# Kernel tuning notes

Measured on AMD Instinct MI355X. Metric: run time of the kernel, lower is better.

## Reference

```python
import jax, jax.numpy as jnp
import numpy as np

B, N, D = 2, 2048, 1024
H, HD = 16, 64            # num_heads, head_dim
INNER = H * HD
EPS = 1e-5


def setup_inputs() -> dict:
    key = jax.random.key(0)
    k0, k1, k2, k3 = jax.random.split(key, 4)
    x = jax.random.normal(k0, (B, N, D), dtype=jnp.float32)
    attn_mask = jax.random.randint(k1, (B, N, N), 0, 2, dtype=jnp.int32)
    gamma = jnp.ones((D,), jnp.float32)
    beta = jnp.zeros((D,), jnp.float32)
    w_qkv = jax.random.normal(k2, (D, 3 * INNER), dtype=jnp.float32) * 0.02
    w_out = jax.random.normal(k3, (INNER, D), dtype=jnp.float32) * 0.02
    b_out = jnp.zeros((D,), jnp.float32)
    return {"x": x, "attn_mask": attn_mask, "gamma": gamma, "beta": beta,
            "w_qkv": w_qkv, "w_out": w_out, "b_out": b_out}


def _rope_tables(n):
    # RotaryEmbedding buffers: sin/cos of shape [n, HD//2]
    inv_freq = 1.0 / (10000.0 ** (jnp.arange(0, HD, 2, dtype=jnp.float32) / HD))
    pos = jnp.arange(n, dtype=jnp.float32)
    ang = pos[:, None] * inv_freq[None, :]          # [n, HD//2]
    return jnp.sin(ang), jnp.cos(ang)


def _apply_rope(t, sin, cos):
    # t: [B, H, N, HD]; sin/cos broadcast as [1, 1, N, HD//2]
    t1, t2 = t[..., : HD // 2], t[..., HD // 2:]
    return jnp.concatenate([t1 * cos - t2 * sin, t2 * cos + t1 * sin], axis=-1)


def reference(x, attn_mask, gamma, beta, w_qkv, w_out, b_out):
    b, n, _ = x.shape
    # LayerNorm
    mu = jnp.mean(x, axis=-1, keepdims=True)
    var = jnp.mean(jnp.square(x - mu), axis=-1, keepdims=True)
    xn = (x - mu) * jax.lax.rsqrt(var + EPS) * gamma + beta
    # QKV projection (no bias)
    qkv = xn @ w_qkv                                 # [B, N, 3*INNER]
    q, k, v = jnp.split(qkv, 3, axis=-1)
    def to_heads(t):
        return t.reshape(b, n, H, HD).transpose(0, 2, 1, 3)  # [B, H, N, HD]
    q, k, v = to_heads(q), to_heads(k), to_heads(v)
    sin, cos = _rope_tables(n)
    sin = sin[None, None]                            # [1,1,N,HD//2]
    cos = cos[None, None]
    q = _apply_rope(q, sin, cos)
    k = _apply_rope(k, sin, cos)
    scale = HD ** -0.5
    scores = jnp.einsum('bhid,bhjd->bhij', q, k) * scale
    mask = (attn_mask > 0)[:, None, :, :]            # [B,1,N,N]
    scores = jnp.where(mask, scores, -jnp.inf)
    probs = jax.nn.softmax(scores, axis=-1)
    probs = jnp.nan_to_num(probs, nan=0.0)           # rows fully masked -> 0
    out = jnp.einsum('bhij,bhjd->bhid', probs, v)    # [B,H,N,HD]
    out = out.transpose(0, 2, 1, 3).reshape(b, n, INNER)
    return out @ w_out + b_out
```

## Files before the change

kernel.cpp:

```cpp
#include <hip/hip_runtime.h>
#include <stdint.h>
#include <math.h>

#define B_ 2
#define N_ 2048
#define D_ 1024
#define H_ 16
#define HD_ 64
#define TOK (B_*N_)
#define INNER_ (H_*HD_)

typedef unsigned short u16;
typedef __attribute__((ext_vector_type(8))) short bf16x8;
typedef __attribute__((ext_vector_type(4))) float f32x4;

__device__ __forceinline__ float bf2f(u16 u) {
  union { uint32_t i; float f; } v; v.i = ((uint32_t)u) << 16; return v.f;
}
__device__ __forceinline__ u16 f2bf(float f) {
  union { uint32_t i; float f; } v; v.f = f;
  uint32_t r = ((v.i >> 16) & 1u) + 0x7fffu;
  return (u16)((v.i + r) >> 16);
}
__device__ __forceinline__ uint32_t pk_bf16(float a, float b) {
  uint32_t ua = __float_as_uint(a) + 0x8000u;
  uint32_t ub = __float_as_uint(b) + 0x8000u;
  return __builtin_amdgcn_perm(ub, ua, 0x07060302);
}
__device__ __forceinline__ void gl_lds16(const void* g, void* l) {
  __builtin_amdgcn_global_load_lds(
      (const __attribute__((address_space(1))) uint32_t*)g,
      (__attribute__((address_space(3))) uint32_t*)l, 16, 0, 0);
}
__device__ __forceinline__ f32x4 mfma16(bf16x8 a, bf16x8 b, f32x4 c) {
  return __builtin_amdgcn_mfma_f32_16x16x32_bf16(a, b, c, 0, 0, 0);
}

__global__ void pack_mask(const int* __restrict__ mask, uint64_t* __restrict__ bits) {
  int t = threadIdx.x, lane = t & 63, w = t >> 6;
  int wi = blockIdx.x * 4 + w;
  int row = wi >> 5, jw = wi & 31;
  int m = mask[(size_t)row * 2048 + jw * 64 + lane];
  uint64_t bm = __ballot(m > 0);
  int b = row >> 11, i = row & 2047;
  if (lane == 0) bits[((size_t)(b * 32 + jw)) * 2048 + i] = bm;
}

__global__ void transpose_f2b(const float* __restrict__ in, u16* __restrict__ out,
                              int R, int C) {
  __shared__ u16 tile[64][65];
  int c0 = blockIdx.x * 64, r0 = blockIdx.y * 64;
  int t = threadIdx.x;
  int c = t & 63, r4 = t >> 6;
  for (int i = 0; i < 16; i++) {
    int r = r4 + i * 4;
    tile[c][r] = f2bf(in[(size_t)(r0 + r) * C + c0 + c]);
  }
  __syncthreads();
  int rr = t & 63, cc4 = t >> 6;
  for (int i = 0; i < 16; i++) {
    int cc = cc4 + i * 4;
    out[(size_t)(c0 + cc) * R + r0 + rr] = tile[cc][rr];
  }
}

__global__ void ln_kernel(const float* __restrict__ x, const float* __restrict__ gamma,
                          const float* __restrict__ beta, u16* __restrict__ xn) {
  int row = blockIdx.x, t = threadIdx.x;
  const float* xr = x + (size_t)row * D_;
  float4 u = *(const float4*)(xr + t * 4);
  float s = u.x + u.y + u.z + u.w;
  float ss = u.x * u.x + u.y * u.y + u.z * u.z + u.w * u.w;
  for (int off = 1; off < 64; off <<= 1) {
    s += __shfl_xor(s, off);
    ss += __shfl_xor(ss, off);
  }
  __shared__ float red[8];
  int wid = t >> 6, lane = t & 63;
  if (lane == 0) { red[wid] = s; red[wid + 4] = ss; }
  __syncthreads();
  s = red[0] + red[1] + red[2] + red[3];
  ss = red[4] + red[5] + red[6] + red[7];
  float mu = s * (1.0f / D_);
  float var = ss * (1.0f / D_) - mu * mu;
  float rinv = rsqrtf(var + 1e-5f);
  float4 g4 = *(const float4*)(gamma + t * 4);
  float4 b4 = *(const float4*)(beta + t * 4);
  ushort4 o;
  o.x = f2bf((u.x - mu) * rinv * g4.x + b4.x);
  o.y = f2bf((u.y - mu) * rinv * g4.y + b4.y);
  o.z = f2bf((u.z - mu) * rinv * g4.z + b4.z);
  o.w = f2bf((u.w - mu) * rinv * g4.w + b4.w);
  *(ushort4*)(xn + (size_t)row * D_ + t * 4) = o;
}

template<int FINAL>
__global__ void gemm_bt(const u16* __restrict__ A, const u16* __restrict__ Bt,
                        void* __restrict__ Cv, const float* __restrict__ bias,
                        int M, int N, int K) {
  __shared__ __align__(16) u16 As[128 * 64];
  __shared__ __align__(16) u16 Bs[128 * 64];
  const int t = threadIdx.x;
  const int lane = t & 63, wid = t >> 6;
  const int m0 = blockIdx.y * 128, n0 = blockIdx.x * 128;
  const int wm = (wid >> 1) * 64, wn = (wid & 1) * 64;
  const int l15 = lane & 15, quad = lane >> 4;

  f32x4 acc[4][4];
  const f32x4 zf = {0.f, 0.f, 0.f, 0.f};
  for (int i = 0; i < 4; i++) for (int j = 0; j < 4; j++) acc[i][j] = zf;

  for (int kb = 0; kb < K; kb += 64) {
    for (int i = 0; i < 4; i++) {
      int e = i * 256 + t;
      int row = e >> 3, gs = e & 7;
      int g = gs ^ (row & 7);
      gl_lds16(A + (size_t)(m0 + row) * K + kb + g * 8, &As[e * 8]);
      gl_lds16(Bt + (size_t)(n0 + row) * K + kb + g * 8, &Bs[e * 8]);
    }
    __syncthreads();
    bf16x8 af[4][2], bfr[4][2];
    for (int mt = 0; mt < 4; mt++)
      for (int kc = 0; kc < 2; kc++) {
        int row = wm + mt * 16 + l15;
        int gs = (kc * 4 + quad) ^ (row & 7);
        af[mt][kc] = *(const bf16x8*)&As[row * 64 + gs * 8];
      }
    for (int nt = 0; nt < 4; nt++)
      for (int kc = 0; kc < 2; kc++) {
        int row = wn + nt * 16 + l15;
        int gs = (kc * 4 + quad) ^ (row & 7);
        bfr[nt][kc] = *(const bf16x8*)&Bs[row * 64 + gs * 8];
      }
    for (int mt = 0; mt < 4; mt++)
      for (int nt = 0; nt < 4; nt++)
        for (int kc = 0; kc < 2; kc++)
          acc[mt][nt] = mfma16(af[mt][kc], bfr[nt][kc], acc[mt][nt]);
    __syncthreads();
  }
  for (int mt = 0; mt < 4; mt++)
    for (int nt = 0; nt < 4; nt++)
      for (int r = 0; r < 4; r++) {
        int row = m0 + wm + mt * 16 + quad * 4 + r;
        int col = n0 + wn + nt * 16 + l15;
        float v = acc[mt][nt][r];
        if (FINAL) {
          ((float*)Cv)[(size_t)row * N + col] = v + bias[col];
        } else {
          ((u16*)Cv)[(size_t)row * N + col] = f2bf(v);
        }
      }
}

__global__ void rope_kernel(const u16* __restrict__ qkv, u16* __restrict__ q,
                            u16* __restrict__ k, u16* __restrict__ vt) {
  int blk = blockIdx.x;
  int nt = blk & 31;
  int h = (blk >> 5) & 15;
  int b = blk >> 9;
  int n0 = nt * 64;
  int t = threadIdx.x;
  __shared__ u16 vs[64][65];
  const float QS = 0.125f * 1.4426950408889634f;
  for (int it = 0; it < 8; it++) {
    int idx = it * 256 + t;
    int i = idx >> 5, p = idx & 31;
    size_t base = (size_t)(b * 2048 + n0 + i) * 3072 + h * 64;
    float q1 = bf2f(qkv[base + p]),        q2 = bf2f(qkv[base + p + 32]);
    float k1 = bf2f(qkv[base + 1024 + p]), k2 = bf2f(qkv[base + 1024 + p + 32]);
    float pos = (float)(n0 + i);
    float inv = exp2f(-(float)p * (13.287712379549449f / 32.0f));
    float ang = pos * inv;
    float sn, cs;
    sincosf(ang, &sn, &cs);
    size_t qo = ((size_t)(b * 16 + h) * 2048 + n0 + i) * 64;
    q[qo + p]      = f2bf((q1 * cs - q2 * sn) * QS);
    q[qo + p + 32] = f2bf((q2 * cs + q1 * sn) * QS);
    k[qo + p]      = f2bf(k1 * cs - k2 * sn);
    k[qo + p + 32] = f2bf(k2 * cs + k1 * sn);
  }
  for (int it = 0; it < 16; it++) {
    int idx = it * 256 + t;
    int i = idx >> 6, d = idx & 63;
    vs[i][d] = qkv[(size_t)(b * 2048 + n0 + i) * 3072 + h * 64 + 2048 + d];
  }
  __syncthreads();
  for (int it = 0; it < 16; it++) {
    int idx = it * 256 + t;
    int d = idx >> 6, i = idx & 63;
    int c = i >> 5, hi = (i >> 4) & 1, qq = (i >> 2) & 3, r = i & 3;
    int slot = c * 32 + qq * 8 + hi * 4 + r;
    vt[((size_t)(b * 16 + h) * 64 + d) * 2048 + n0 + slot] = vs[i][d];
  }
}

__global__ __launch_bounds__(256, 4)
void attn_kernel(const u16* __restrict__ q, const u16* __restrict__ k,
                 const u16* __restrict__ vt, const uint64_t* __restrict__ bitsT,
                 u16* __restrict__ out) {
  int blk = blockIdx.x;
  int qt = blk & 31;
  int bh = blk >> 5;
  int b = bh >> 4, h = bh & 15;
  int q0 = qt * 64;
  int t = threadIdx.x, lane = t & 63, w = t >> 6;
  int l15 = lane & 15, quad = lane >> 4;

  __shared__ __align__(16) u16 sQ[64 * 64];
  __shared__ __align__(16) u16 sK[2][64 * 64];
  __shared__ __align__(16) u16 sV[2][64 * 64];

  {
    int e0 = t, e1 = 256 + t;
    int r0 = e0 >> 3, g0 = (e0 & 7) ^ (r0 & 7);
    int r1 = e1 >> 3, g1 = (e1 & 7) ^ (r1 & 7);
    gl_lds16(q + ((size_t)bh * 2048 + q0 + r0) * 64 + g0 * 8, &sQ[e0 * 8]);
    gl_lds16(q + ((size_t)bh * 2048 + q0 + r1) * 64 + g1 * 8, &sQ[e1 * 8]);
    gl_lds16(k + ((size_t)bh * 2048 + r0) * 64 + g0 * 8, &sK[0][e0 * 8]);
    gl_lds16(k + ((size_t)bh * 2048 + r1) * 64 + g1 * 8, &sK[0][e1 * 8]);
    gl_lds16(vt + ((size_t)bh * 64 + r0) * 2048 + g0 * 8, &sV[0][e0 * 8]);
    gl_lds16(vt + ((size_t)bh * 64 + r1) * 2048 + g1 * 8, &sV[0][e1 * 8]);
  }
  __syncthreads();

  bf16x8 bq[2];
  {
    int row = w * 16 + l15;
    for (int kc = 0; kc < 2; kc++) {
      int gs = (kc * 4 + quad) ^ (row & 7);
      bq[kc] = *(const bf16x8*)&sQ[row * 64 + gs * 8];
    }
  }

  const f32x4 zf = {0.f, 0.f, 0.f, 0.f};
  float l_i = 0.f;
  f32x4 acc_o[4];
  for (int dt = 0; dt < 4; dt++) acc_o[dt] = zf;
  const int qrow = q0 + w * 16 + l15;

  #pragma unroll 2
  for (int j64 = 0; j64 < 32; j64++) {
    if (j64) __syncthreads();
    int cur = j64 & 1;
    if (j64 + 1 < 32) {
      int nxt = cur ^ 1, j0n = (j64 + 1) * 64;
      int e0 = t, e1 = 256 + t;
      int r0 = e0 >> 3, g0 = (e0 & 7) ^ (r0 & 7);
      int r1 = e1 >> 3, g1 = (e1 & 7) ^ (r1 & 7);
      gl_lds16(k + ((size_t)bh * 2048 + j0n + r0) * 64 + g0 * 8, &sK[nxt][e0 * 8]);
      gl_lds16(k + ((size_t)bh * 2048 + j0n + r1) * 64 + g1 * 8, &sK[nxt][e1 * 8]);
      gl_lds16(vt + ((size_t)bh * 64 + r0) * 2048 + j0n + g0 * 8, &sV[nxt][e0 * 8]);
      gl_lds16(vt + ((size_t)bh * 64 + r1) * 2048 + j0n + g1 * 8, &sV[nxt][e1 * 8]);
    }
    const u16* sKc = sK[cur];
    const u16* sVc = sV[cur];

    uint64_t word = bitsT[((size_t)(b * 32 + j64)) * 2048 + qrow];
    uint64_t sh = word >> (quad * 4);
    uint32_t mlo = (uint32_t)sh, mhi = (uint32_t)(sh >> 32);

    float p[16];
    {
      f32x4 st[4];
      for (int jt = 0; jt < 4; jt++) {
        st[jt] = zf;
        int row = jt * 16 + l15;
        for (int kc = 0; kc < 2; kc++) {
          int gs = (kc * 4 + quad) ^ (row & 7);
          bf16x8 ak = *(const bf16x8*)&sKc[row * 64 + gs * 8];
          st[jt] = mfma16(ak, bq[kc], st[jt]);
        }
      }
      for (int jt = 0; jt < 4; jt++) {
        uint32_t mw = (jt & 2) ? mhi : mlo;
        int base = (jt & 1) * 16;
        for (int r = 0; r < 4; r++) {
          bool on = (mw >> (base + r)) & 1u;
          float e = exp2f(st[jt][r]);
          p[jt * 4 + r] = on ? e : 0.f;
        }
      }
    }
    float rsum = 0.f;
    for (int i = 0; i < 16; i++) rsum += p[i];
    rsum += __shfl_xor(rsum, 16);
    rsum += __shfl_xor(rsum, 32);
    l_i += rsum;

    for (int c = 0; c < 2; c++) {
      union { bf16x8 v; uint32_t d[4]; } bp;
      bp.d[0] = pk_bf16(p[(2 * c) * 4 + 0], p[(2 * c) * 4 + 1]);
      bp.d[1] = pk_bf16(p[(2 * c) * 4 + 2], p[(2 * c) * 4 + 3]);
      bp.d[2] = pk_bf16(p[(2 * c + 1) * 4 + 0], p[(2 * c + 1) * 4 + 1]);
      bp.d[3] = pk_bf16(p[(2 * c + 1) * 4 + 2], p[(2 * c + 1) * 4 + 3]);
      for (int dt = 0; dt < 4; dt++) {
        int drow = dt * 16 + l15;
        int gpos = (4 * c + quad) ^ (drow & 7);
        bf16x8 av = *(const bf16x8*)&sVc[drow * 64 + gpos * 8];
        acc_o[dt] = mfma16(av, bp.v, acc_o[dt]);
      }
    }
  }
  float rl = (l_i > 0.f) ? 1.0f / l_i : 0.f;
  size_t obase = ((size_t)b * 2048 + qrow) * 1024 + h * 64;
  for (int dt = 0; dt < 4; dt++) {
    ushort4 o;
    o.x = f2bf(acc_o[dt][0] * rl);
    o.y = f2bf(acc_o[dt][1] * rl);
    o.z = f2bf(acc_o[dt][2] * rl);
    o.w = f2bf(acc_o[dt][3] * rl);
    *(ushort4*)&out[obase + dt * 16 + quad * 4] = o;
  }
}

extern "C" void kernel_launch(void* const* d_in, const int* in_sizes, int n_in,
                              void* d_out, int out_size, void* d_ws, size_t ws_size,
                              hipStream_t stream) {
  const float* x = (const float*)d_in[0];
  const int* mask = (const int*)d_in[1];
  const float* gamma = (const float*)d_in[2];
  const float* beta = (const float*)d_in[3];
  const float* wqkv = (const float*)d_in[4];
  const float* wout = (const float*)d_in[5];
  const float* bout = (const float*)d_in[6];
  float* out = (float*)d_out;

  uint8_t* ws = (uint8_t*)d_ws;
  size_t o = 0;
  uint64_t* mbits = (uint64_t*)(ws + o); o += (size_t)TOK * 32 * 8;
  u16* wqkvT = (u16*)(ws + o); o += (size_t)3 * INNER_ * D_ * 2;
  u16* woutT = (u16*)(ws + o); o += (size_t)INNER_ * D_ * 2;
  u16* xn    = (u16*)(ws + o); o += (size_t)TOK * D_ * 2;
  u16* qkv   = (u16*)(ws + o); o += (size_t)TOK * 3 * INNER_ * 2;
  u16* kb    = (u16*)(ws + o); o += (size_t)TOK * INNER_ * 2;
  u16* vtb   = (u16*)(ws + o); o += (size_t)TOK * INNER_ * 2;
  u16* qb = xn;
  u16* ao = qkv;

  pack_mask<<<TOK * 32 / 4, 256, 0, stream>>>(mask, mbits);
  transpose_f2b<<<dim3(3 * INNER_ / 64, D_ / 64), 256, 0, stream>>>(wqkv, wqkvT, D_, 3 * INNER_);
  transpose_f2b<<<dim3(D_ / 64, INNER_ / 64), 256, 0, stream>>>(wout, woutT, INNER_, D_);
  ln_kernel<<<TOK, 256, 0, stream>>>(x, gamma, beta, xn);
  gemm_bt<0><<<dim3(3 * INNER_ / 128, TOK / 128), 256, 0, stream>>>(xn, wqkvT, qkv, nullptr, TOK, 3 * INNER_, D_);
  rope_kernel<<<B_ * H_ * (N_ / 64), 256, 0, stream>>>(qkv, qb, kb, vtb);
  attn_kernel<<<B_ * H_ * (N_ / 64), 256, 0, stream>>>(qb, kb, vtb, mbits, ao);
  gemm_bt<1><<<dim3(D_ / 128, TOK / 128), 256, 0, stream>>>(ao, woutT, out, bout, TOK, D_, INNER_);
}
```

Before: 257.3 us.

## Fuse RoPE and V transpose into QKV GEMM epilogue, double-buffer output GEMM

```diff
diff --git a/kernel.cpp b/kernel.cpp
--- a/kernel.cpp
+++ b/kernel.cpp
@@ -22,7 +22,10 @@
   uint32_t r = ((v.i >> 16) & 1u) + 0x7fffu;
   return (u16)((v.i + r) >> 16);
 }
-__device__ __forceinline__ uint32_t pk_bf16(float a, float b) {
+__device__ __forceinline__ uint32_t pk_trunc(float a, float b) {
+  return __builtin_amdgcn_perm(__float_as_uint(b), __float_as_uint(a), 0x07060302);
+}
+__device__ __forceinline__ uint32_t pk_rnd(float a, float b) {
   uint32_t ua = __float_as_uint(a) + 0x8000u;
   uint32_t ub = __float_as_uint(b) + 0x8000u;
   return __builtin_amdgcn_perm(ub, ua, 0x07060302);
@@ -38,12 +41,25 @@
 
 __global__ void pack_mask(const int* __restrict__ mask, uint64_t* __restrict__ bits) {
   int t = threadIdx.x, lane = t & 63, w = t >> 6;
-  int wi = blockIdx.x * 4 + w;
-  int row = wi >> 5, jw = wi & 31;
-  int m = mask[(size_t)row * 2048 + jw * 64 + lane];
-  uint64_t bm = __ballot(m > 0);
+  int seg = blockIdx.x * 4 + w;
+  int row = seg >> 3, s = seg & 7;
+  const int* mp = mask + (size_t)row * 2048 + s * 256;
   int b = row >> 11, i = row & 2047;
-  if (lane == 0) bits[((size_t)(b * 32 + jw)) * 2048 + i] = bm;
+  uint64_t* bp = bits + (size_t)b * 32 * 2048 + i;
+  for (int j = 0; j < 4; j++) {
+    int m = mp[j * 64 + lane];
+    uint64_t bm = __ballot(m > 0);
+    if (lane == 0) bp[(size_t)(s * 4 + j) * 2048] = bm;
+  }
+}
+
+__global__ void rtab_kernel(float2* __restrict__ rtab) {
+  int i = blockIdx.x * 256 + threadIdx.x;
+  int pos = i >> 5, p = i & 31;
+  float inv = exp2f(-(float)p * (13.287712379549449f / 32.0f));
+  float sn, cs;
+  sincosf((float)pos * inv, &sn, &cs);
+  rtab[i] = make_float2(sn, cs);
 }
 
 __global__ void transpose_f2b(const float* __restrict__ in, u16* __restrict__ out,
@@ -94,10 +110,11 @@
   *(ushort4*)(xn + (size_t)row * D_ + t * 4) = o;
 }
 
-template<int FINAL>
-__global__ void gemm_bt(const u16* __restrict__ A, const u16* __restrict__ Bt,
-                        void* __restrict__ Cv, const float* __restrict__ bias,
-                        int M, int N, int K) {
+__global__ void gemm_qkv(const u16* __restrict__ A, const u16* __restrict__ Bt,
+                         const float2* __restrict__ rtab,
+                         u16* __restrict__ q, u16* __restrict__ k,
+                         u16* __restrict__ vt) {
+  const int K = 1024;
   __shared__ __align__(16) u16 As[128 * 64];
   __shared__ __align__(16) u16 Bs[128 * 64];
   const int t = threadIdx.x;
@@ -138,60 +155,107 @@
           acc[mt][nt] = mfma16(af[mt][kc], bfr[nt][kc], acc[mt][nt]);
     __syncthreads();
   }
+
+  const int sec = n0 >> 10;
+  const int h = ((n0 & 1023) >> 6) + (wn >> 6);
+  if (sec < 2) {
+    u16* dst = sec ? k : q;
+    const float scale = sec ? 1.0f : 0.125f * 1.4426950408889634f;
+    for (int mt = 0; mt < 4; mt++)
+      for (int r = 0; r < 4; r++) {
+        int row = m0 + wm + mt * 16 + quad * 4 + r;
+        int b = row >> 11, pos = row & 2047;
+        float2 c0 = rtab[pos * 32 + l15];
+        float2 c1 = rtab[pos * 32 + 16 + l15];
+        float a0 = acc[mt][0][r], a1 = acc[mt][1][r];
+        float a2 = acc[mt][2][r], a3 = acc[mt][3][r];
+        float o0 = (a0 * c0.y - a2 * c0.x) * scale;
+        float o2 = (a2 * c0.y + a0 * c0.x) * scale;
+        float o1 = (a1 * c1.y - a3 * c1.x) * scale;
+        float o3 = (a3 * c1.y + a1 * c1.x) * scale;
+        size_t base = ((size_t)(b * 16 + h) * 2048 + pos) * 64;
+        dst[base + l15]      = f2bf(o0);
+        dst[base + 16 + l15] = f2bf(o1);
+        dst[base + 32 + l15] = f2bf(o2);
+        dst[base + 48 + l15] = f2bf(o3);
+      }
+  } else {
+    for (int mt = 0; mt < 4; mt++) {
+      int u = (wm + mt * 16) >> 4;
+      int c = (u >> 1) & 1, hi = u & 1;
+      int rowb = m0 + (u >> 2) * 64;
+      int b = rowb >> 11, nb = rowb & 2047;
+      int slot = nb + c * 32 + quad * 8 + hi * 4;
+      for (int nt = 0; nt < 4; nt++) {
+        int d = nt * 16 + l15;
+        size_t base = ((size_t)(b * 16 + h) * 64 + d) * 2048 + slot;
+        uint2 o;
+        o.x = pk_rnd(acc[mt][nt][0], acc[mt][nt][1]);
+        o.y = pk_rnd(acc[mt][nt][2], acc[mt][nt][3]);
+        *(uint2*)&vt[base] = o;
+      }
+    }
+  }
+}
+
+__global__ void gemm_out(const u16* __restrict__ A, const u16* __restrict__ Bt,
+                         float* __restrict__ C, const float* __restrict__ bias) {
+  const int N = 1024, K = 1024;
+  __shared__ __align__(16) u16 As[2][128 * 64];
+  __shared__ __align__(16) u16 Bs[2][128 * 64];
+  const int t = threadIdx.x;
+  const int lane = t & 63, wid = t >> 6;
+  const int m0 = blockIdx.y * 128, n0 = blockIdx.x * 128;
+  const int wm = (wid >> 1) * 64, wn = (wid & 1) * 64;
+  const int l15 = lane & 15, quad = lane >> 4;
+
+  f32x4 acc[4][4];
+  const f32x4 zf = {0.f, 0.f, 0.f, 0.f};
+  for (int i = 0; i < 4; i++) for (int j = 0; j < 4; j++) acc[i][j] = zf;
+
+  for (int i = 0; i < 4; i++) {
+    int e = i * 256 + t;
+    int row = e >> 3, gs = e & 7, g = gs ^ (row & 7);
+    gl_lds16(A + (size_t)(m0 + row) * K + g * 8, &As[0][e * 8]);
+    gl_lds16(Bt + (size_t)(n0 + row) * K + g * 8, &Bs[0][e * 8]);
+  }
+  for (int ki = 0; ki < 16; ki++) {
+    int cur = ki & 1;
+    __syncthreads();
+    if (ki + 1 < 16) {
+      int nxt = cur ^ 1, kb = (ki + 1) * 64;
+      for (int i = 0; i < 4; i++) {
+        int e = i * 256 + t;
+        int row = e >> 3, gs = e & 7, g = gs ^ (row & 7);
+        gl_lds16(A + (size_t)(m0 + row) * K + kb + g * 8, &As[nxt][e * 8]);
+        gl_lds16(Bt + (size_t)(n0 + row) * K + kb + g * 8, &Bs[nxt][e * 8]);
+      }
+    }
+    bf16x8 af[4][2], bfr[4][2];
+    for (int mt = 0; mt < 4; mt++)
+      for (int kc = 0; kc < 2; kc++) {
+        int row = wm + mt * 16 + l15;
+        int gs = (kc * 4 + quad) ^ (row & 7);
+        af[mt][kc] = *(const bf16x8*)&As[cur][row * 64 + gs * 8];
+      }
+    for (int nt = 0; nt < 4; nt++)
+      for (int kc = 0; kc < 2; kc++) {
+        int row = wn + nt * 16 + l15;
+        int gs = (kc * 4 + quad) ^ (row & 7);
+        bfr[nt][kc] = *(const bf16x8*)&Bs[cur][row * 64 + gs * 8];
+      }
+    for (int mt = 0; mt < 4; mt++)
+      for (int nt = 0; nt < 4; nt++)
+        for (int kc = 0; kc < 2; kc++)
+          acc[mt][nt] = mfma16(af[mt][kc], bfr[nt][kc], acc[mt][nt]);
+  }
   for (int mt = 0; mt < 4; mt++)
     for (int nt = 0; nt < 4; nt++)
       for (int r = 0; r < 4; r++) {
         int row = m0 + wm + mt * 16 + quad * 4 + r;
         int col = n0 + wn + nt * 16 + l15;
-        float v = acc[mt][nt][r];
-        if (FINAL) {
-          ((float*)Cv)[(size_t)row * N + col] = v + bias[col];
-        } else {
-          ((u16*)Cv)[(size_t)row * N + col] = f2bf(v);
-        }
-      }
-}
-
-__global__ void rope_kernel(const u16* __restrict__ qkv, u16* __restrict__ q,
-                            u16* __restrict__ k, u16* __restrict__ vt) {
-  int blk = blockIdx.x;
-  int nt = blk & 31;
-  int h = (blk >> 5) & 15;
-  int b = blk >> 9;
-  int n0 = nt * 64;
-  int t = threadIdx.x;
-  __shared__ u16 vs[64][65];
-  const float QS = 0.125f * 1.4426950408889634f;
-  for (int it = 0; it < 8; it++) {
-    int idx = it * 256 + t;
-    int i = idx >> 5, p = idx & 31;
-    size_t base = (size_t)(b * 2048 + n0 + i) * 3072 + h * 64;
-    float q1 = bf2f(qkv[base + p]),        q2 = bf2f(qkv[base + p + 32]);
-    float k1 = bf2f(qkv[base + 1024 + p]), k2 = bf2f(qkv[base + 1024 + p + 32]);
-    float pos = (float)(n0 + i);
-    float inv = exp2f(-(float)p * (13.287712379549449f / 32.0f));
-    float ang = pos * inv;
-    float sn, cs;
-    sincosf(ang, &sn, &cs);
-    size_t qo = ((size_t)(b * 16 + h) * 2048 + n0 + i) * 64;
-    q[qo + p]      = f2bf((q1 * cs - q2 * sn) * QS);
-    q[qo + p + 32] = f2bf((q2 * cs + q1 * sn) * QS);
-    k[qo + p]      = f2bf(k1 * cs - k2 * sn);
-    k[qo + p + 32] = f2bf(k2 * cs + k1 * sn);
-  }
-  for (int it = 0; it < 16; it++) {
-    int idx = it * 256 + t;
-    int i = idx >> 6, d = idx & 63;
-    vs[i][d] = qkv[(size_t)(b * 2048 + n0 + i) * 3072 + h * 64 + 2048 + d];
-  }
-  __syncthreads();
-  for (int it = 0; it < 16; it++) {
-    int idx = it * 256 + t;
-    int d = idx >> 6, i = idx & 63;
-    int c = i >> 5, hi = (i >> 4) & 1, qq = (i >> 2) & 3, r = i & 3;
-    int slot = c * 32 + qq * 8 + hi * 4 + r;
-    vt[((size_t)(b * 16 + h) * 64 + d) * 2048 + n0 + slot] = vs[i][d];
-  }
+        C[(size_t)row * N + col] = acc[mt][nt][r] + bias[col];
+      }
 }
 
 __global__ __launch_bounds__(256, 4)
@@ -289,10 +353,10 @@
 
     for (int c = 0; c < 2; c++) {
       union { bf16x8 v; uint32_t d[4]; } bp;
-      bp.d[0] = pk_bf16(p[(2 * c) * 4 + 0], p[(2 * c) * 4 + 1]);
-      bp.d[1] = pk_bf16(p[(2 * c) * 4 + 2], p[(2 * c) * 4 + 3]);
-      bp.d[2] = pk_bf16(p[(2 * c + 1) * 4 + 0], p[(2 * c + 1) * 4 + 1]);
-      bp.d[3] = pk_bf16(p[(2 * c + 1) * 4 + 2], p[(2 * c + 1) * 4 + 3]);
+      bp.d[0] = pk_trunc(p[(2 * c) * 4 + 0], p[(2 * c) * 4 + 1]);
+      bp.d[1] = pk_trunc(p[(2 * c) * 4 + 2], p[(2 * c) * 4 + 3]);
+      bp.d[2] = pk_trunc(p[(2 * c + 1) * 4 + 0], p[(2 * c + 1) * 4 + 1]);
+      bp.d[3] = pk_trunc(p[(2 * c + 1) * 4 + 2], p[(2 * c + 1) * 4 + 3]);
       for (int dt = 0; dt < 4; dt++) {
         int drow = dt * 16 + l15;
         int gpos = (4 * c + quad) ^ (drow & 7);
@@ -331,18 +395,18 @@
   u16* wqkvT = (u16*)(ws + o); o += (size_t)3 * INNER_ * D_ * 2;
   u16* woutT = (u16*)(ws + o); o += (size_t)INNER_ * D_ * 2;
   u16* xn    = (u16*)(ws + o); o += (size_t)TOK * D_ * 2;
-  u16* qkv   = (u16*)(ws + o); o += (size_t)TOK * 3 * INNER_ * 2;
+  u16* qb    = (u16*)(ws + o); o += (size_t)TOK * INNER_ * 2;
   u16* kb    = (u16*)(ws + o); o += (size_t)TOK * INNER_ * 2;
   u16* vtb   = (u16*)(ws + o); o += (size_t)TOK * INNER_ * 2;
-  u16* qb = xn;
-  u16* ao = qkv;
-
-  pack_mask<<<TOK * 32 / 4, 256, 0, stream>>>(mask, mbits);
+  u16* ao    = (u16*)(ws + o); o += (size_t)TOK * INNER_ * 2;
+  float2* rtab = (float2*)(ws + o); o += (size_t)2048 * 32 * 8;
+
+  pack_mask<<<8192, 256, 0, stream>>>(mask, mbits);
+  rtab_kernel<<<256, 256, 0, stream>>>(rtab);
   transpose_f2b<<<dim3(3 * INNER_ / 64, D_ / 64), 256, 0, stream>>>(wqkv, wqkvT, D_, 3 * INNER_);
   transpose_f2b<<<dim3(D_ / 64, INNER_ / 64), 256, 0, stream>>>(wout, woutT, INNER_, D_);
   ln_kernel<<<TOK, 256, 0, stream>>>(x, gamma, beta, xn);
-  gemm_bt<0><<<dim3(3 * INNER_ / 128, TOK / 128), 256, 0, stream>>>(xn, wqkvT, qkv, nullptr, TOK, 3 * INNER_, D_);
-  rope_kernel<<<B_ * H_ * (N_ / 64), 256, 0, stream>>>(qkv, qb, kb, vtb);
+  gemm_qkv<<<dim3(3 * INNER_ / 128, TOK / 128), 256, 0, stream>>>(xn, wqkvT, rtab, qb, kb, vtb);
   attn_kernel<<<B_ * H_ * (N_ / 64), 256, 0, stream>>>(qb, kb, vtb, mbits, ao);
-  gemm_bt<1><<<dim3(D_ / 128, TOK / 128), 256, 0, stream>>>(ao, woutT, out, bout, TOK, D_, INNER_);
-}
+  gemm_out<<<dim3(D_ / 128, TOK / 128), 256, 0, stream>>>(ao, woutT, out, bout);
+}
```

After: 247.2 us. 1.04x faster.
